# Kernel tuning notes

Hardware: AMD Instinct MI355X
Metric: run time of the kernel (lower is better)

Reference implementation:

```python
import jax, jax.numpy as jnp
import numpy as np

N, E, IN_DIM, H, OUT, MAPD = 20000, 640000, 24, 128, 24, 512
SLOPE = 0.01  # torch F.leaky_relu default


def setup_inputs() -> dict:
    key = jax.random.key(0)
    ks = jax.random.split(key, 20)
    g = lambda i, shape, s: jax.random.normal(ks[i], shape, jnp.float32) * s
    inp = {
        "feats": g(0, (N, IN_DIM), 1.0),
        "e_w": jax.random.uniform(ks[1], (E, 1), dtype=jnp.float32),
        "maps_embedding": g(2, (N, MAPD), 1.0),
        "snorm_n": jnp.ones((N, 1), jnp.float32),
        "src": jax.random.randint(ks[3], (E,), 0, N),
        "dst": jax.random.randint(ks[4], (E,), 0, N),
        "W_eh": g(5, (H, IN_DIM), (2.0 / IN_DIM) ** 0.5), "b_eh": jnp.zeros((H,), jnp.float32),
        "W_ee": g(6, (H, 1), 1.0), "b_ee": jnp.zeros((H,), jnp.float32),
        "W_cat": g(7, (H, H + MAPD), (2.0 / (H + MAPD)) ** 0.5), "b_cat": jnp.zeros((H,), jnp.float32),
        "Ws1": g(8, (H, H), (2.0 / H) ** 0.5), "Wf1": g(9, (H, H), (2.0 / H) ** 0.5),
        "a1": g(10, (2 * H,), (2.0 / (2 * H)) ** 0.5),
        "Ws2": g(11, (H, H), (2.0 / H) ** 0.5), "Wf2": g(12, (H, H), (2.0 / H) ** 0.5),
        "a2": g(13, (2 * H,), (2.0 / (2 * H)) ** 0.5),
        "W_out": g(14, (OUT, H), (2.0 / H) ** 0.5), "b_out": jnp.zeros((OUT,), jnp.float32),
    }
    return inp


def gat_layer(h, src, dst, Ws, Wf, a):
    # My_GATLayer with (as constructed in My_GAT) relu=False, att_ew=False, dropouts=0.
    h_in = h
    h_s = h @ Ws.T                         # [N,H] self transform
    z = h @ Wf.T                           # [N,H] message transform
    # attention score = leaky_relu(a^T [z_src, z_dst]) computed via per-node halves
    s_src = z @ a[:H]                      # [N]
    s_dst = z @ a[H:]                      # [N]
    e = jax.nn.leaky_relu(s_src[src] + s_dst[dst], SLOPE)          # [E]
    # numerically stable segment softmax over incoming edges grouped by dst
    m = jax.ops.segment_max(e, dst, num_segments=N)
    m = jnp.where(jnp.isfinite(m), m, 0.0)
    ex = jnp.exp(e - m[dst])
    denom = jax.ops.segment_sum(ex, dst, num_segments=N)
    alpha = ex / jnp.maximum(denom[dst], 1e-16)                    # [E]
    agg = jax.ops.segment_sum(alpha[:, None] * z[src], dst, num_segments=N)  # [N,H]
    indeg = jax.ops.segment_sum(jnp.ones_like(e), dst, num_segments=N)
    # DGL update_all leaves zero-in-degree nodes at their prior ndata['h'] (= h_in)
    h_node = jnp.where(indeg[:, None] > 0, h_s + agg, h_in)
    return h_in + h_node                   # residual connection; relu disabled (positional-arg bug)


def reference(feats, e_w, maps_embedding, snorm_n, src, dst,
              W_eh, b_eh, W_ee, b_ee, W_cat, b_cat,
              Ws1, Wf1, a1, Ws2, Wf2, a2, W_out, b_out):
    feats = feats.reshape(feats.shape[0], -1)
    h = feats @ W_eh.T + b_eh                                  # embedding_h
    _e = e_w @ W_ee.T + b_ee                                   # edge embedding (stored on g.edata['w'], unused since att_ew binds to attn_drop)
    h = jnp.concatenate([maps_embedding, h], axis=-1) @ W_cat.T + b_cat
    h = jax.nn.relu(h)
    h = gat_layer(h, src, dst, Ws1, Wf1, a1)
    h = gat_layer(h, src, dst, Ws2, Wf2, a2)
    return h @ W_out.T + b_out
```

## Files before the change

### kernel.cpp

```cpp
#include <hip/hip_runtime.h>

#define HBLK 128
#define EPB 4096

typedef __attribute__((ext_vector_type(8))) short s8v;
typedef __attribute__((ext_vector_type(4))) float f32x4;
typedef __attribute__((ext_vector_type(8))) _Float16 h8f;

__device__ inline void split2(float x, short& h, short& l) {
    unsigned hb = __float_as_uint(x) & 0xFFFF0000u;
    float hf = __uint_as_float(hb);
    float lf = x - hf;
    h = (short)(hb >> 16);
    l = (short)(__float_as_uint(lf) >> 16);
}

__device__ inline void split8(const float4& a0, const float4& a1, s8v& ah, s8v& al) {
    float vv[8];
    *(float4*)&vv[0] = a0;
    *(float4*)&vv[4] = a1;
#pragma unroll
    for (int e = 0; e < 8; ++e) {
        short hh, ll;
        split2(vv[e], hh, ll);
        ah[e] = hh;
        al[e] = ll;
    }
}


__global__ void bin_hist(const int* __restrict__ dst, int* __restrict__ histT,
                         int E, int NB1) {
    __shared__ int h[256];
    const int t = threadIdx.x, blk = blockIdx.x;
    h[t] = 0;
    __syncthreads();
    const int e0 = blk * EPB;
    const int e1 = min(E, e0 + EPB);
    for (int e = e0 + t; e < e1; e += 256)
        atomicAdd(&h[dst[e] >> 7], 1);
    __syncthreads();
    histT[t * NB1 + blk] = h[t];
}

__global__ void scan1(const int* __restrict__ counts, int* __restrict__ offs,
                      int* __restrict__ bsums, int n) {
    __shared__ int lds[256];
    const int t = threadIdx.x;
    const int i = blockIdx.x * 256 + t;
    const int v = (i < n) ? counts[i] : 0;
    lds[t] = v;
    __syncthreads();
    for (int off = 1; off < 256; off <<= 1) {
        int add = (t >= off) ? lds[t - off] : 0;
        __syncthreads();
        lds[t] += add;
        __syncthreads();
    }
    if (i < n) offs[i] = lds[t] - v;
    if (t == 255) bsums[blockIdx.x] = lds[255];
}

__global__ void scan2(int* __restrict__ bsums, int nb) {
    __shared__ int lds[256];
    const int t = threadIdx.x;
    const int v = (t < nb) ? bsums[t] : 0;
    lds[t] = v;
    __syncthreads();
    for (int off = 1; off < 256; off <<= 1) {
        int add = (t >= off) ? lds[t - off] : 0;
        __syncthreads();
        lds[t] += add;
        __syncthreads();
    }
    if (t < nb) bsums[t] = lds[t] - v;
}

__global__ void bin_scatter(const int* __restrict__ src, const int* __restrict__ dst,
                            const int* __restrict__ histT, const int* __restrict__ bsums,
                            int* __restrict__ ebuf, int E, int NB1) {
    __shared__ int cur[256];
    const int t = threadIdx.x, blk = blockIdx.x;
    const int li = t * NB1 + blk;
    cur[t] = histT[li] + bsums[li >> 8];
    __syncthreads();
    const int e0 = blk * EPB;
    const int e1 = min(E, e0 + EPB);
    for (int e = e0 + t; e < e1; e += 256) {
        const int d = dst[e];
        const int p = atomicAdd(&cur[d >> 7], 1);
        ebuf[p] = (src[e] << 7) | (d & 127);
    }
}

__global__ void bucket_sort(const int* __restrict__ ebuf, const int* __restrict__ histT,
                            const int* __restrict__ bsums,
                            int* __restrict__ offs, int* __restrict__ srcs,
                            int N, int E, int NB1) {
    __shared__ int cnt[256];
    __shared__ int cur[256];
    const int t = threadIdx.x, b = blockIdx.x;
    const int li0 = b * NB1;
    const int ebase = histT[li0] + bsums[li0 >> 8];
    int eend = E;
    if (b + 1 < 256) {
        const int li1 = (b + 1) * NB1;
        eend = histT[li1] + bsums[li1 >> 8];
    }
    cnt[t] = 0;
    __syncthreads();
    for (int e = ebase + t; e < eend; e += 256)
        atomicAdd(&cnt[ebuf[e] & 127], 1);
    __syncthreads();
    const int own = cnt[t];
    for (int off = 1; off < 256; off <<= 1) {
        int add = (t >= off) ? cnt[t - off] : 0;
        __syncthreads();
        cnt[t] += add;
        __syncthreads();
    }
    const int excl = cnt[t] - own;
    cur[t] = ebase + excl;
    const int node = (b << 7) + t;
    if (t < 128 && node < N) offs[node] = ebase + excl;
    if (b == 0 && t == 0) offs[N] = E;
    __syncthreads();
    for (int e = ebase + t; e < eend; e += 256) {
        const int ed = ebuf[e];
        const int p = atomicAdd(&cur[ed & 127], 1);
        srcs[p] = ed >> 7;
    }
}

__global__ void pack_all(const float* __restrict__ W0, const float* __restrict__ W1,
                         const float* __restrict__ W2, const float* __restrict__ W3,
                         short* __restrict__ dh, short* __restrict__ dl,
                         const float* __restrict__ Wcat, int ldw, int mapd,
                         const float* __restrict__ Weh, int indim,
                         const float* __restrict__ beh, const float* __restrict__ bcat,
                         short* __restrict__ ch, short* __restrict__ cl,
                         float* __restrict__ bcomb, int K) {
    const int m = blockIdx.y;
    const long i = (long)blockIdx.x * 256 + threadIdx.x;
    if (m < 4) {
        if (blockIdx.x >= 64) return;
        const float* Ws[4] = {W0, W1, W2, W3};
        const int c = (int)(i >> 7), k = (int)(i & 127);
        float x = Ws[m][c * HBLK + k];
        short h, l;
        split2(x, h, l);
        const int j = c >> 4, l16 = c & 15;
        const int chunk = k >> 5, quad = (k >> 3) & 3, t = k & 7;
        const long off = (long)m * 16384 + (((long)(chunk * 8 + j) * 64) + quad * 16 + l16) * 8 + t;
        dh[off] = h;
        dl[off] = l;
    } else {
        const long total = (long)HBLK * K;
        if (i < total) {
            const int c = (int)(i / K), k = (int)(i % K);
            float x = 0.f;
            if (k < mapd) {
                x = Wcat[(long)c * ldw + k];
            } else if (k < mapd + indim) {
                const float* wc = Wcat + (long)c * ldw + mapd;
                const int kk = k - mapd;
                float s = 0.f;
                for (int j = 0; j < HBLK; ++j) s += wc[j] * Weh[j * indim + kk];
                x = s;
            }
            short h, l;
            split2(x, h, l);
            const int j = c >> 4, l16 = c & 15;
            const int chunk = k >> 5, quad = (k >> 3) & 3, t = k & 7;
            const long off = (((long)(chunk * 8 + j) * 64) + quad * 16 + l16) * 8 + t;
            ch[off] = h;
            cl[off] = l;
        } else if (i < total + HBLK) {
            const int c = (int)(i - total);
            const float* wc = Wcat + (long)c * ldw + mapd;
            float s = bcat[c];
            for (int j = 0; j < HBLK; ++j) s += wc[j] * beh[j];
            bcomb[c] = s;
        }
    }
}

__global__ __launch_bounds__(256, 2) void gemm_bigk(
    const float* __restrict__ A1, int lda1, int K1,
    const float* __restrict__ A2, int lda2, int Kin,
    int K,
    const short* __restrict__ Wh, const short* __restrict__ Wl,
    const float* __restrict__ bias,
    float* __restrict__ Cf, int M)
{
    __shared__ short lds_h[2][4096];
    __shared__ short lds_l[2][4096];
    const int tid = threadIdx.x;
    const int wv = tid >> 6;
    const int lane = tid & 63;
    const int l16 = lane & 15;
    const int quad = lane >> 4;
    const int m0 = blockIdx.x * 64 + wv * 16;
    int ra = m0 + l16;
    if (ra >= M) ra = M - 1;
    const long r1 = (long)ra * lda1;
    const long r2 = (long)ra * lda2;
    const int NC = K >> 5;

    f32x4 acc[8];
#pragma unroll
    for (int j = 0; j < 8; ++j) acc[j] = (f32x4){0.f, 0.f, 0.f, 0.f};

#define LOAD_A(d0, d1, kb)                                      \
    {                                                           \
        const int col0 = (kb) + quad * 8;                       \
        if (col0 < K1) {                                        \
            const float* ap = A1 + r1 + col0;                   \
            d0 = *(const float4*)ap;                            \
            d1 = *(const float4*)(ap + 4);                      \
        } else if (col0 < Kin) {                                \
            const float* ap = A2 + r2 + (col0 - K1);            \
            d0 = *(const float4*)ap;                            \
            d1 = *(const float4*)(ap + 4);                      \
        } else {                                                \
            d0 = make_float4(0.f, 0.f, 0.f, 0.f);               \
            d1 = make_float4(0.f, 0.f, 0.f, 0.f);               \
        }                                                       \
    }
#define LOAD_W(r0, r1w, r2w, r3, c)                             \
    {                                                           \
        const int4* gh = (const int4*)(Wh + (long)(c) * 4096);  \
        const int4* gl = (const int4*)(Wl + (long)(c) * 4096);  \
        r0 = gh[tid * 2]; r1w = gh[tid * 2 + 1];                \
        r2w = gl[tid * 2]; r3 = gl[tid * 2 + 1];                \
    }
#define WRITE_W(b, r0, r1w, r2w, r3)                            \
    {                                                           \
        int4* bh = (int4*)lds_h[b];                             \
        int4* bl = (int4*)lds_l[b];                             \
        bh[tid * 2] = r0; bh[tid * 2 + 1] = r1w;                \
        bl[tid * 2] = r2w; bl[tid * 2 + 1] = r3;                \
    }

    int4 wa0, wa1, wa2, wa3, wb0, wb1, wb2, wb3;
    LOAD_W(wa0, wa1, wa2, wa3, 0)
    WRITE_W(0, wa0, wa1, wa2, wa3)
    LOAD_W(wa0, wa1, wa2, wa3, 1)
    LOAD_W(wb0, wb1, wb2, wb3, 2)
    float4 a0c, a1c, a0n, a1n, a0p, a1p;
    float4 a0q = make_float4(0.f, 0.f, 0.f, 0.f);
    float4 a1q = make_float4(0.f, 0.f, 0.f, 0.f);
    LOAD_A(a0c, a1c, 0)
    LOAD_A(a0n, a1n, 32)
    LOAD_A(a0p, a1p, 64)
    asm volatile("s_waitcnt lgkmcnt(0)" ::: "memory");
    __builtin_amdgcn_s_barrier();
    asm volatile("" ::: "memory");

    for (int c = 0; c < NC; ++c) {
        const int nb = c & 1;
        if (c + 3 < NC) {
            LOAD_A(a0q, a1q, (c + 3) * 32)
        }
        s8v ah, al;
        split8(a0c, a1c, ah, al);
#pragma unroll
        for (int j = 0; j < 8; ++j) {
            const s8v whf = *(const s8v*)&lds_h[nb][(j * 64 + lane) * 8];
            const s8v wlf = *(const s8v*)&lds_l[nb][(j * 64 + lane) * 8];
            acc[j] = __builtin_amdgcn_mfma_f32_16x16x32_bf16(ah, whf, acc[j], 0, 0, 0);
            acc[j] = __builtin_amdgcn_mfma_f32_16x16x32_bf16(ah, wlf, acc[j], 0, 0, 0);
            acc[j] = __builtin_amdgcn_mfma_f32_16x16x32_bf16(al, whf, acc[j], 0, 0, 0);
        }
        if (c + 1 < NC) {
            WRITE_W(nb ^ 1, wa0, wa1, wa2, wa3)
            wa0 = wb0; wa1 = wb1; wa2 = wb2; wa3 = wb3;
            if (c + 3 < NC) LOAD_W(wb0, wb1, wb2, wb3, c + 3)
            asm volatile("s_waitcnt lgkmcnt(0)" ::: "memory");
            __builtin_amdgcn_s_barrier();
            asm volatile("" ::: "memory");
        }
        a0c = a0n; a1c = a1n;
        a0n = a0p; a1n = a1p;
        a0p = a0q; a1p = a1q;
    }
#undef LOAD_A
#undef LOAD_W
#undef WRITE_W

#pragma unroll
    for (int r = 0; r < 4; ++r) {
        const int gr = m0 + quad * 4 + r;
        if (gr >= M) continue;
#pragma unroll
        for (int j = 0; j < 8; ++j) {
            const int col = j * 16 + l16;
            float v = acc[j][r] + bias[col];
            Cf[(long)gr * HBLK + col] = fmaxf(v, 0.f);
        }
    }
}

__global__ __launch_bounds__(256, 2) void gemm_layer(
    const float* __restrict__ A,
    const short* __restrict__ Wsh, const short* __restrict__ Wsl,
    const short* __restrict__ Wfh, const short* __restrict__ Wfl,
    float* __restrict__ hsOut, _Float16* __restrict__ zOut,
    const float* __restrict__ avec,
    float* __restrict__ sOut, float* __restrict__ dOut, int M)
{
    __shared__ short lh[16384];
    __shared__ short ll[16384];
    const int tid = threadIdx.x;
    const int wv = tid >> 6;
    const int lane = tid & 63;
    const int l16 = lane & 15;
    const int quad = lane >> 4;
    const int m0 = blockIdx.x * 64 + wv * 16;
    int ra = m0 + l16;
    if (ra >= M) ra = M - 1;
    const float* arow = A + (long)ra * HBLK + quad * 8;

    {
        const int4* gh = (const int4*)Wfh;
        const int4* gl = (const int4*)Wfl;
        int4* bh = (int4*)lh;
        int4* bl = (int4*)ll;
#pragma unroll
        for (int i = 0; i < 8; ++i) {
            bh[i * 256 + tid] = gh[i * 256 + tid];
            bl[i * 256 + tid] = gl[i * 256 + tid];
        }
    }
    float4 aw0[4], aw1[4];
#pragma unroll
    for (int c = 0; c < 4; ++c) {
        aw0[c] = *(const float4*)(arow + c * 32);
        aw1[c] = *(const float4*)(arow + c * 32 + 4);
    }
    int4 wsh[8], wsl[8];
    {
        const int4* gh = (const int4*)Wsh;
        const int4* gl = (const int4*)Wsl;
#pragma unroll
        for (int i = 0; i < 8; ++i) {
            wsh[i] = gh[i * 256 + tid];
            wsl[i] = gl[i * 256 + tid];
        }
    }
    s8v ahf[4], alf[4];
#pragma unroll
    for (int c = 0; c < 4; ++c) split8(aw0[c], aw1[c], ahf[c], alf[c]);

    f32x4 acc[8];
#pragma unroll
    for (int j = 0; j < 8; ++j) acc[j] = (f32x4){0.f, 0.f, 0.f, 0.f};
    asm volatile("s_waitcnt lgkmcnt(0)" ::: "memory");
    __builtin_amdgcn_s_barrier();
    asm volatile("" ::: "memory");

#pragma unroll
    for (int c = 0; c < 4; ++c) {
#pragma unroll
        for (int j = 0; j < 8; ++j) {
            const s8v whf = *(const s8v*)&lh[((c * 8 + j) * 64 + lane) * 8];
            const s8v wlf = *(const s8v*)&ll[((c * 8 + j) * 64 + lane) * 8];
            acc[j] = __builtin_amdgcn_mfma_f32_16x16x32_bf16(ahf[c], whf, acc[j], 0, 0, 0);
            acc[j] = __builtin_amdgcn_mfma_f32_16x16x32_bf16(ahf[c], wlf, acc[j], 0, 0, 0);
            acc[j] = __builtin_amdgcn_mfma_f32_16x16x32_bf16(alf[c], whf, acc[j], 0, 0, 0);
        }
    }
#pragma unroll
    for (int r = 0; r < 4; ++r) {
        const int gr = m0 + quad * 4 + r;
        if (gr >= M) continue;
#pragma unroll
        for (int j = 0; j < 8; ++j)
            zOut[(long)gr * HBLK + j * 16 + l16] = (_Float16)acc[j][r];
    }
    {
        float av0[8], av1[8];
#pragma unroll
        for (int j = 0; j < 8; ++j) {
            av0[j] = avec[j * 16 + l16];
            av1[j] = avec[128 + j * 16 + l16];
        }
#pragma unroll
        for (int r = 0; r < 4; ++r) {
            float ssp = 0.f, sdp = 0.f;
#pragma unroll
            for (int j = 0; j < 8; ++j) {
                const float v = acc[j][r];
                ssp += v * av0[j];
                sdp += v * av1[j];
            }
#pragma unroll
            for (int off = 1; off < 16; off <<= 1) {
                ssp += __shfl_xor(ssp, off);
                sdp += __shfl_xor(sdp, off);
            }
            const int gr = m0 + quad * 4 + r;
            if (l16 == 0 && gr < M) {
                sOut[gr] = ssp;
                dOut[gr] = sdp;
            }
        }
    }

    asm volatile("s_waitcnt lgkmcnt(0)" ::: "memory");
    __builtin_amdgcn_s_barrier();
    asm volatile("" ::: "memory");
    {
        int4* bh = (int4*)lh;
        int4* bl = (int4*)ll;
#pragma unroll
        for (int i = 0; i < 8; ++i) {
            bh[i * 256 + tid] = wsh[i];
            bl[i * 256 + tid] = wsl[i];
        }
    }
    asm volatile("s_waitcnt lgkmcnt(0)" ::: "memory");
    __builtin_amdgcn_s_barrier();
    asm volatile("" ::: "memory");

#pragma unroll
    for (int j = 0; j < 8; ++j) acc[j] = (f32x4){0.f, 0.f, 0.f, 0.f};
#pragma unroll
    for (int c = 0; c < 4; ++c) {
#pragma unroll
        for (int j = 0; j < 8; ++j) {
            const s8v whf = *(const s8v*)&lh[((c * 8 + j) * 64 + lane) * 8];
            const s8v wlf = *(const s8v*)&ll[((c * 8 + j) * 64 + lane) * 8];
            acc[j] = __builtin_amdgcn_mfma_f32_16x16x32_bf16(ahf[c], whf, acc[j], 0, 0, 0);
            acc[j] = __builtin_amdgcn_mfma_f32_16x16x32_bf16(ahf[c], wlf, acc[j], 0, 0, 0);
            acc[j] = __builtin_amdgcn_mfma_f32_16x16x32_bf16(alf[c], whf, acc[j], 0, 0, 0);
        }
    }
#pragma unroll
    for (int r = 0; r < 4; ++r) {
        const int gr = m0 + quad * 4 + r;
        if (gr >= M) continue;
#pragma unroll
        for (int j = 0; j < 8; ++j)
            hsOut[(long)gr * HBLK + j * 16 + l16] = acc[j][r];
    }
}

template <int FOUT>
__global__ void gat_gather(const float* __restrict__ h_in, const float* __restrict__ hs,
                           const _Float16* __restrict__ zh,
                           const float* __restrict__ s_src, const float* __restrict__ s_dst,
                           const int* __restrict__ offs, const int* __restrict__ srcs,
                           float* __restrict__ h_out,
                           const float* __restrict__ Wout, const float* __restrict__ bout,
                           float* __restrict__ outp, int OUTD, int N) {
    __shared__ float wlds[FOUT ? (32 * 132 + 4 * 132) : 4];
    const int tid = threadIdx.x;
    const int wave = tid >> 6;
    const int lane = tid & 63;
    if constexpr (FOUT) {
        for (int i = tid; i < OUTD * HBLK; i += 256)
            wlds[(i >> 7) * 132 + (i & 127)] = Wout[i];
        __syncthreads();
    }
    const int n = blockIdx.x * 4 + wave;
    if (n >= N) return;
    const int g = lane >> 4, l = lane & 15;
    const int beg = offs[n], end = offs[n + 1];
    const int deg = end - beg;

    float acc[8] = {};
    if (deg > 0) {
        const float sd = s_dst[n];
        if (deg <= 64) {
            const int sA = srcs[beg + min(lane, deg - 1)];
            float e = sd + s_src[sA];
            e = e > 0.f ? e : 0.01f * e;
            if (lane >= deg) e = -INFINITY;
            float mv = e;
#pragma unroll
            for (int off = 32; off; off >>= 1) mv = fmaxf(mv, __shfl_xor(mv, off));
            const float ex = (lane < deg) ? __expf(e - mv) : 0.f;
            float sv = ex;
#pragma unroll
            for (int off = 32; off; off >>= 1) sv += __shfl_xor(sv, off);
            const float w = ex / fmaxf(sv, 1e-16f);

            const int nK = (deg + 3) >> 2;
            int k = 0;
            for (; k + 1 < nK; k += 2) {
                const int i0 = 4 * k + g;
                const int i1 = i0 + 4;
                const int s0 = __shfl(sA, i0);
                const int s1 = __shfl(sA, i1);
                const float w0 = __shfl(w, i0);
                const float w1 = __shfl(w, i1);
                const h8f z0 = *(const h8f*)(zh + (long)s0 * HBLK + 8 * l);
                const h8f z1 = *(const h8f*)(zh + (long)s1 * HBLK + 8 * l);
#pragma unroll
                for (int e2 = 0; e2 < 8; ++e2)
                    acc[e2] += w0 * (float)z0[e2] + w1 * (float)z1[e2];
            }
            if (k < nK) {
                const int i0 = 4 * k + g;
                const int s0 = __shfl(sA, i0);
                const float w0 = __shfl(w, i0);
                const h8f z0 = *(const h8f*)(zh + (long)s0 * HBLK + 8 * l);
#pragma unroll
                for (int e2 = 0; e2 < 8; ++e2)
                    acc[e2] += w0 * (float)z0[e2];
            }
        } else {
            float m = -INFINITY, s = 0.f;
            for (int i = beg + lane; i < end; i += 64) {
                float e = sd + s_src[srcs[i]];
                e = e > 0.f ? e : 0.01f * e;
                float nm = fmaxf(m, e);
                s = s * __expf(m - nm) + __expf(e - nm);
                m = nm;
            }
#pragma unroll
            for (int off = 32; off > 0; off >>= 1) {
                float m2 = __shfl_down(m, off);
                float s2 = __shfl_down(s, off);
                if (m2 > m) {
                    float t = m; m = m2; m2 = t;
                    float ts = s; s = s2; s2 = ts;
                }
                s = (m == -INFINITY) ? 0.f : s + s2 * __expf(m2 - m);
            }
            m = __shfl(m, 0);
            s = __shfl(s, 0);
            const float inv = 1.f / fmaxf(s, 1e-16f);
            for (int i = beg + g; i < end; i += 4) {
                const int s0 = srcs[i];
                float e0 = sd + s_src[s0];
                e0 = e0 > 0.f ? e0 : 0.01f * e0;
                const float w0 = __expf(e0 - m) * inv;
                const h8f z0 = *(const h8f*)(zh + (long)s0 * HBLK + 8 * l);
#pragma unroll
                for (int e2 = 0; e2 < 8; ++e2)
                    acc[e2] += w0 * (float)z0[e2];
            }
        }
#pragma unroll
        for (int e2 = 0; e2 < 8; ++e2) {
            acc[e2] += __shfl_down(acc[e2], 32);
            acc[e2] += __shfl_down(acc[e2], 16);
        }
    }

    if (g == 0) {
        const long base = (long)n * HBLK + 8 * l;
        const float4 hi0 = *(const float4*)(h_in + base);
        const float4 hi1 = *(const float4*)(h_in + base + 4);
        float o[8];
        if (deg > 0) {
            const float4 hv0 = *(const float4*)(hs + base);
            const float4 hv1 = *(const float4*)(hs + base + 4);
            const float* hip = (const float*)&hi0;
            const float* hvp = (const float*)&hv0;
#pragma unroll
            for (int e = 0; e < 4; ++e) o[e] = hip[e] + hvp[e] + acc[e];
            const float* hip1 = (const float*)&hi1;
            const float* hvp1 = (const float*)&hv1;
#pragma unroll
            for (int e = 0; e < 4; ++e) o[4 + e] = hip1[e] + hvp1[e] + acc[4 + e];
        } else {
            const float* hip = (const float*)&hi0;
            const float* hip1 = (const float*)&hi1;
#pragma unroll
            for (int e = 0; e < 4; ++e) o[e] = 2.f * hip[e];
#pragma unroll
            for (int e = 0; e < 4; ++e) o[4 + e] = 2.f * hip1[e];
        }
        if constexpr (FOUT) {
            float* hr = wlds + 32 * 132 + wave * 132;
            *(float4*)&hr[8 * l] = *(float4*)&o[0];
            *(float4*)&hr[8 * l + 4] = *(float4*)&o[4];
        } else {
            *(float4*)(h_out + base) = *(float4*)&o[0];
            *(float4*)(h_out + base + 4) = *(float4*)&o[4];
        }
    }
    if constexpr (FOUT) {
        if (lane < OUTD) {
            const float* hr = wlds + 32 * 132 + wave * 132;
            const float* wr = wlds + lane * 132;
            float a = bout[lane];
#pragma unroll 8
            for (int k = 0; k < 32; ++k) {
                const float4 hv = *(const float4*)&hr[k * 4];
                const float4 wv = *(const float4*)&wr[k * 4];
                a += hv.x * wv.x + hv.y * wv.y + hv.z * wv.z + hv.w * wv.w;
            }
            outp[(long)n * OUTD + lane] = a;
        }
    }
}

extern "C" void kernel_launch(void* const* d_in, const int* in_sizes, int n_in,
                              void* d_out, int out_size, void* d_ws, size_t ws_size,
                              hipStream_t stream) {
    const float* feats = (const float*)d_in[0];
    const float* maps  = (const float*)d_in[2];
    const int* src = (const int*)d_in[4];
    const int* dst = (const int*)d_in[5];
    const float* W_eh  = (const float*)d_in[6];
    const float* b_eh  = (const float*)d_in[7];
    const float* W_cat = (const float*)d_in[10];
    const float* b_cat = (const float*)d_in[11];
    const float* Ws1 = (const float*)d_in[12];
    const float* Wf1 = (const float*)d_in[13];
    const float* a1  = (const float*)d_in[14];
    const float* Ws2 = (const float*)d_in[15];
    const float* Wf2 = (const float*)d_in[16];
    const float* a2  = (const float*)d_in[17];
    const float* W_out = (const float*)d_in[18];
    const float* b_out = (const float*)d_in[19];

    const int N = in_sizes[3];
    const int E = in_sizes[4];
    const int IN_DIM = in_sizes[0] / N;
    const int MAPD = in_sizes[2] / N;
    const int OUTD = in_sizes[19];
    const int KCAT = MAPD + HBLK;
    const int KC = (MAPD + IN_DIM + 31) & ~31;

    char* p = (char*)d_ws;
    const size_t NH = (size_t)N * HBLK;
    float* hin  = (float*)p;  p += NH * 4;
    float* hs   = (float*)p;  p += NH * 4;
    float* hout = (float*)p;  p += NH * 4;
    _Float16* zh = (_Float16*)p; p += NH * 2;
    float* ssrc = (float*)p;  p += (size_t)N * 4;
    float* sdst = (float*)p;  p += (size_t)N * 4;
    int* offs   = (int*)p;    p += (size_t)(N + 1) * 4;
    int* srcs   = (int*)p;    p += (size_t)E * 4;
    int* bsums  = (int*)p;    p += 256 * 4;
    int* histT  = (int*)p;    p += (size_t)256 * 256 * 4;
    float* bcomb = (float*)p; p += (size_t)HBLK * 4;
    p = (char*)(((uintptr_t)p + 15) & ~(uintptr_t)15);
    int* ebuf = (int*)p;      p += (size_t)E * 4;
    short* Wcat_h = (short*)p; p += (size_t)HBLK * KC * 2;
    short* Wcat_l = (short*)p; p += (size_t)HBLK * KC * 2;
    short* Wly_h = (short*)p;  p += (size_t)4 * HBLK * HBLK * 2;
    short* Wly_l = (short*)p;  p += (size_t)4 * HBLK * HBLK * 2;

    const int NB1 = (E + EPB - 1) / EPB;
    const int NBUCK = (N + 127) >> 7;
    const int nHist = 256 * NB1;
    bin_hist<<<NB1, 256, 0, stream>>>(dst, histT, E, NB1);
    scan1<<<NB1, 256, 0, stream>>>(histT, histT, bsums, nHist);
    scan2<<<1, 256, 0, stream>>>(bsums, NB1);
    bin_scatter<<<NB1, 256, 0, stream>>>(src, dst, histT, bsums, ebuf, E, NB1);
    bucket_sort<<<NBUCK, 256, 0, stream>>>(ebuf, histT, bsums, offs, srcs, N, E, NB1);

    const int nbW = (HBLK * KC + HBLK + 255) / 256;
    pack_all<<<dim3(nbW, 5), 256, 0, stream>>>(
        Ws1, Wf1, Ws2, Wf2, Wly_h, Wly_l,
        W_cat, KCAT, MAPD, W_eh, IN_DIM, b_eh, b_cat, Wcat_h, Wcat_l, bcomb, KC);

    const int gGrid = (N + 63) / 64;
    const int n4 = (N + 3) / 4;

    gemm_bigk<<<gGrid, 256, 0, stream>>>(
        maps, MAPD, MAPD, feats, IN_DIM, MAPD + IN_DIM, KC,
        Wcat_h, Wcat_l, bcomb, hin, N);

    gemm_layer<<<gGrid, 256, 0, stream>>>(
        hin, Wly_h, Wly_l, Wly_h + 16384, Wly_l + 16384,
        hs, zh, a1, ssrc, sdst, N);
    gat_gather<0><<<n4, 256, 0, stream>>>(hin, hs, zh, ssrc, sdst, offs, srcs, hout,
                                          nullptr, nullptr, nullptr, OUTD, N);

    gemm_layer<<<gGrid, 256, 0, stream>>>(
        hout, Wly_h + 32768, Wly_l + 32768, Wly_h + 49152, Wly_l + 49152,
        hs, zh, a2, ssrc, sdst, N);
    gat_gather<1><<<n4, 256, 0, stream>>>(hout, hs, zh, ssrc, sdst, offs, srcs, nullptr,
                                          W_out, b_out, (float*)d_out, OUTD, N);
}
```

Baseline: 261.2 us.

## Merge CSR build and weight packing into one cooperative kernel with grid syncs

Replaces the five CSR-construction kernels and the weight-pack kernel with a single cooperative launch of 256 blocks that uses grid.sync between phases. Weight packing runs in the blocks not needed for the histogram, so the two overlap. This removes several kernel launches and their gaps, at the cost of grid-wide barriers and a fixed grid of 256 blocks that must all be co-resident.

```diff
diff --git a/kernel.cpp b/kernel.cpp
--- a/kernel.cpp
+++ b/kernel.cpp
@@ -1,4 +1,7 @@
 #include <hip/hip_runtime.h>
+#include <hip/hip_cooperative_groups.h>
+
+namespace cg = cooperative_groups;
 
 #define HBLK 128
 #define EPB 4096
@@ -29,158 +32,157 @@
 }
 
 
-__global__ void bin_hist(const int* __restrict__ dst, int* __restrict__ histT,
-                         int E, int NB1) {
-    __shared__ int h[256];
+struct CoopArgs {
+    const int* src; const int* dst;
+    int* histT; int* bsums; int* ebuf; int* offs; int* srcs;
+    int E; int N; int NB1; int NBUCK;
+    const float* W0; const float* W1; const float* W2; const float* W3;
+    short* dh; short* dl;
+    const float* Wcat; int ldw; int mapd;
+    const float* Weh; int indim;
+    const float* beh; const float* bcat;
+    short* ch; short* cl; float* bcomb; int K;
+};
+
+__global__ __launch_bounds__(256, 1) void csr_pack_coop(CoopArgs a) {
+    cg::grid_group grid = cg::this_grid();
+    __shared__ int sh0[256];
+    __shared__ int sh1[256];
     const int t = threadIdx.x, blk = blockIdx.x;
-    h[t] = 0;
-    __syncthreads();
-    const int e0 = blk * EPB;
-    const int e1 = min(E, e0 + EPB);
-    for (int e = e0 + t; e < e1; e += 256)
-        atomicAdd(&h[dst[e] >> 7], 1);
-    __syncthreads();
-    histT[t * NB1 + blk] = h[t];
-}
-
-__global__ void scan1(const int* __restrict__ counts, int* __restrict__ offs,
-                      int* __restrict__ bsums, int n) {
-    __shared__ int lds[256];
-    const int t = threadIdx.x;
-    const int i = blockIdx.x * 256 + t;
-    const int v = (i < n) ? counts[i] : 0;
-    lds[t] = v;
-    __syncthreads();
-    for (int off = 1; off < 256; off <<= 1) {
-        int add = (t >= off) ? lds[t - off] : 0;
-        __syncthreads();
-        lds[t] += add;
-        __syncthreads();
-    }
-    if (i < n) offs[i] = lds[t] - v;
-    if (t == 255) bsums[blockIdx.x] = lds[255];
-}
-
-__global__ void scan2(int* __restrict__ bsums, int nb) {
-    __shared__ int lds[256];
-    const int t = threadIdx.x;
-    const int v = (t < nb) ? bsums[t] : 0;
-    lds[t] = v;
-    __syncthreads();
-    for (int off = 1; off < 256; off <<= 1) {
-        int add = (t >= off) ? lds[t - off] : 0;
-        __syncthreads();
-        lds[t] += add;
-        __syncthreads();
-    }
-    if (t < nb) bsums[t] = lds[t] - v;
-}
-
-__global__ void bin_scatter(const int* __restrict__ src, const int* __restrict__ dst,
-                            const int* __restrict__ histT, const int* __restrict__ bsums,
-                            int* __restrict__ ebuf, int E, int NB1) {
-    __shared__ int cur[256];
-    const int t = threadIdx.x, blk = blockIdx.x;
-    const int li = t * NB1 + blk;
-    cur[t] = histT[li] + bsums[li >> 8];
-    __syncthreads();
-    const int e0 = blk * EPB;
-    const int e1 = min(E, e0 + EPB);
-    for (int e = e0 + t; e < e1; e += 256) {
-        const int d = dst[e];
-        const int p = atomicAdd(&cur[d >> 7], 1);
-        ebuf[p] = (src[e] << 7) | (d & 127);
-    }
-}
-
-__global__ void bucket_sort(const int* __restrict__ ebuf, const int* __restrict__ histT,
-                            const int* __restrict__ bsums,
-                            int* __restrict__ offs, int* __restrict__ srcs,
-                            int N, int E, int NB1) {
-    __shared__ int cnt[256];
-    __shared__ int cur[256];
-    const int t = threadIdx.x, b = blockIdx.x;
-    const int li0 = b * NB1;
-    const int ebase = histT[li0] + bsums[li0 >> 8];
-    int eend = E;
-    if (b + 1 < 256) {
-        const int li1 = (b + 1) * NB1;
-        eend = histT[li1] + bsums[li1 >> 8];
-    }
-    cnt[t] = 0;
-    __syncthreads();
-    for (int e = ebase + t; e < eend; e += 256)
-        atomicAdd(&cnt[ebuf[e] & 127], 1);
-    __syncthreads();
-    const int own = cnt[t];
-    for (int off = 1; off < 256; off <<= 1) {
-        int add = (t >= off) ? cnt[t - off] : 0;
-        __syncthreads();
-        cnt[t] += add;
-        __syncthreads();
-    }
-    const int excl = cnt[t] - own;
-    cur[t] = ebase + excl;
-    const int node = (b << 7) + t;
-    if (t < 128 && node < N) offs[node] = ebase + excl;
-    if (b == 0 && t == 0) offs[N] = E;
-    __syncthreads();
-    for (int e = ebase + t; e < eend; e += 256) {
-        const int ed = ebuf[e];
-        const int p = atomicAdd(&cur[ed & 127], 1);
-        srcs[p] = ed >> 7;
-    }
-}
-
-__global__ void pack_all(const float* __restrict__ W0, const float* __restrict__ W1,
-                         const float* __restrict__ W2, const float* __restrict__ W3,
-                         short* __restrict__ dh, short* __restrict__ dl,
-                         const float* __restrict__ Wcat, int ldw, int mapd,
-                         const float* __restrict__ Weh, int indim,
-                         const float* __restrict__ beh, const float* __restrict__ bcat,
-                         short* __restrict__ ch, short* __restrict__ cl,
-                         float* __restrict__ bcomb, int K) {
-    const int m = blockIdx.y;
-    const long i = (long)blockIdx.x * 256 + threadIdx.x;
-    if (m < 4) {
-        if (blockIdx.x >= 64) return;
-        const float* Ws[4] = {W0, W1, W2, W3};
-        const int c = (int)(i >> 7), k = (int)(i & 127);
-        float x = Ws[m][c * HBLK + k];
-        short h, l;
-        split2(x, h, l);
-        const int j = c >> 4, l16 = c & 15;
-        const int chunk = k >> 5, quad = (k >> 3) & 3, t = k & 7;
-        const long off = (long)m * 16384 + (((long)(chunk * 8 + j) * 64) + quad * 16 + l16) * 8 + t;
-        dh[off] = h;
-        dl[off] = l;
+
+    if (blk < a.NB1) {
+        sh0[t] = 0;
+        __syncthreads();
+        const int e0 = blk * EPB, e1 = min(a.E, e0 + EPB);
+        for (int e = e0 + t; e < e1; e += 256)
+            atomicAdd(&sh0[a.dst[e] >> 7], 1);
+        __syncthreads();
+        a.histT[t * a.NB1 + blk] = sh0[t];
     } else {
-        const long total = (long)HBLK * K;
-        if (i < total) {
-            const int c = (int)(i / K), k = (int)(i % K);
-            float x = 0.f;
-            if (k < mapd) {
-                x = Wcat[(long)c * ldw + k];
-            } else if (k < mapd + indim) {
-                const float* wc = Wcat + (long)c * ldw + mapd;
-                const int kk = k - mapd;
-                float s = 0.f;
-                for (int j = 0; j < HBLK; ++j) s += wc[j] * Weh[j * indim + kk];
-                x = s;
-            }
-            short h, l;
-            split2(x, h, l);
-            const int j = c >> 4, l16 = c & 15;
-            const int chunk = k >> 5, quad = (k >> 3) & 3, t = k & 7;
-            const long off = (((long)(chunk * 8 + j) * 64) + quad * 16 + l16) * 8 + t;
-            ch[off] = h;
-            cl[off] = l;
-        } else if (i < total + HBLK) {
-            const int c = (int)(i - total);
-            const float* wc = Wcat + (long)c * ldw + mapd;
-            float s = bcat[c];
-            for (int j = 0; j < HBLK; ++j) s += wc[j] * beh[j];
-            bcomb[c] = s;
+        const int pb = blk - a.NB1, npb = 256 - a.NB1;
+        const long tw = 65536 + (long)HBLK * a.K + HBLK;
+        for (long idx = (long)pb * 256 + t; idx < tw; idx += (long)npb * 256) {
+            if (idx < 65536) {
+                const int m = (int)(idx >> 14);
+                const long i = idx & 16383;
+                const float* W = (m == 0) ? a.W0 : (m == 1) ? a.W1 : (m == 2) ? a.W2 : a.W3;
+                const int c = (int)(i >> 7), k = (int)(i & 127);
+                float x = W[c * HBLK + k];
+                short h, l;
+                split2(x, h, l);
+                const int j = c >> 4, l16 = c & 15;
+                const int chunk = k >> 5, quad = (k >> 3) & 3, tt = k & 7;
+                const long off = (long)m * 16384 +
+                                 (((long)(chunk * 8 + j) * 64) + quad * 16 + l16) * 8 + tt;
+                a.dh[off] = h;
+                a.dl[off] = l;
+            } else {
+                const long i = idx - 65536;
+                const long total = (long)HBLK * a.K;
+                if (i < total) {
+                    const int c = (int)(i / a.K), k = (int)(i % a.K);
+                    float x = 0.f;
+                    if (k < a.mapd) {
+                        x = a.Wcat[(long)c * a.ldw + k];
+                    } else if (k < a.mapd + a.indim) {
+                        const float* wc = a.Wcat + (long)c * a.ldw + a.mapd;
+                        const int kk = k - a.mapd;
+                        float s = 0.f;
+                        for (int j = 0; j < HBLK; ++j) s += wc[j] * a.Weh[j * a.indim + kk];
+                        x = s;
+                    }
+                    short h, l;
+                    split2(x, h, l);
+                    const int j = c >> 4, l16 = c & 15;
+                    const int chunk = k >> 5, quad = (k >> 3) & 3, tt = k & 7;
+                    const long off = (((long)(chunk * 8 + j) * 64) + quad * 16 + l16) * 8 + tt;
+                    a.ch[off] = h;
+                    a.cl[off] = l;
+                } else {
+                    const int c = (int)(i - total);
+                    const float* wc = a.Wcat + (long)c * a.ldw + a.mapd;
+                    float s = a.bcat[c];
+                    for (int j = 0; j < HBLK; ++j) s += wc[j] * a.beh[j];
+                    a.bcomb[c] = s;
+                }
+            }
+        }
+    }
+    grid.sync();
+
+    if (blk < a.NB1) {
+        const int i = blk * 256 + t;
+        const int v = a.histT[i];
+        sh0[t] = v;
+        __syncthreads();
+        for (int off = 1; off < 256; off <<= 1) {
+            int add = (t >= off) ? sh0[t - off] : 0;
+            __syncthreads();
+            sh0[t] += add;
+            __syncthreads();
+        }
+        a.histT[i] = sh0[t] - v;
+        if (t == 255) a.bsums[blk] = sh0[255];
+    }
+    grid.sync();
+
+    if (blk == 0) {
+        const int v = (t < a.NB1) ? a.bsums[t] : 0;
+        sh0[t] = v;
+        __syncthreads();
+        for (int off = 1; off < 256; off <<= 1) {
+            int add = (t >= off) ? sh0[t - off] : 0;
+            __syncthreads();
+            sh0[t] += add;
+            __syncthreads();
+        }
+        if (t < a.NB1) a.bsums[t] = sh0[t] - v;
+    }
+    grid.sync();
+
+    if (blk < a.NB1) {
+        const int li = t * a.NB1 + blk;
+        sh0[t] = a.histT[li] + a.bsums[li >> 8];
+        __syncthreads();
+        const int e0 = blk * EPB, e1 = min(a.E, e0 + EPB);
+        for (int e = e0 + t; e < e1; e += 256) {
+            const int d = a.dst[e];
+            const int p = atomicAdd(&sh0[d >> 7], 1);
+            a.ebuf[p] = (a.src[e] << 7) | (d & 127);
+        }
+    }
+    grid.sync();
+
+    if (blk < a.NBUCK) {
+        const int li0 = blk * a.NB1;
+        const int ebase = a.histT[li0] + a.bsums[li0 >> 8];
+        int eend = a.E;
+        if (blk + 1 < 256) {
+            const int li1 = (blk + 1) * a.NB1;
+            eend = a.histT[li1] + a.bsums[li1 >> 8];
+        }
+        sh0[t] = 0;
+        __syncthreads();
+        for (int e = ebase + t; e < eend; e += 256)
+            atomicAdd(&sh0[a.ebuf[e] & 127], 1);
+        __syncthreads();
+        const int own = sh0[t];
+        for (int off = 1; off < 256; off <<= 1) {
+            int add = (t >= off) ? sh0[t - off] : 0;
+            __syncthreads();
+            sh0[t] += add;
+            __syncthreads();
+        }
+        const int excl = sh0[t] - own;
+        sh1[t] = ebase + excl;
+        const int node = (blk << 7) + t;
+        if (t < 128 && node < a.N) a.offs[node] = ebase + excl;
+        if (blk == 0 && t == 0) a.offs[a.N] = a.E;
+        __syncthreads();
+        for (int e = ebase + t; e < eend; e += 256) {
+            const int ed = a.ebuf[e];
+            const int p = atomicAdd(&sh1[ed & 127], 1);
+            a.srcs[p] = ed >> 7;
         }
     }
 }
@@ -649,17 +651,19 @@
 
     const int NB1 = (E + EPB - 1) / EPB;
     const int NBUCK = (N + 127) >> 7;
-    const int nHist = 256 * NB1;
-    bin_hist<<<NB1, 256, 0, stream>>>(dst, histT, E, NB1);
-    scan1<<<NB1, 256, 0, stream>>>(histT, histT, bsums, nHist);
-    scan2<<<1, 256, 0, stream>>>(bsums, NB1);
-    bin_scatter<<<NB1, 256, 0, stream>>>(src, dst, histT, bsums, ebuf, E, NB1);
-    bucket_sort<<<NBUCK, 256, 0, stream>>>(ebuf, histT, bsums, offs, srcs, N, E, NB1);
-
-    const int nbW = (HBLK * KC + HBLK + 255) / 256;
-    pack_all<<<dim3(nbW, 5), 256, 0, stream>>>(
-        Ws1, Wf1, Ws2, Wf2, Wly_h, Wly_l,
-        W_cat, KCAT, MAPD, W_eh, IN_DIM, b_eh, b_cat, Wcat_h, Wcat_l, bcomb, KC);
+    CoopArgs ca;
+    ca.src = src; ca.dst = dst;
+    ca.histT = histT; ca.bsums = bsums; ca.ebuf = ebuf; ca.offs = offs; ca.srcs = srcs;
+    ca.E = E; ca.N = N; ca.NB1 = NB1; ca.NBUCK = NBUCK;
+    ca.W0 = Ws1; ca.W1 = Wf1; ca.W2 = Ws2; ca.W3 = Wf2;
+    ca.dh = Wly_h; ca.dl = Wly_l;
+    ca.Wcat = W_cat; ca.ldw = KCAT; ca.mapd = MAPD;
+    ca.Weh = W_eh; ca.indim = IN_DIM;
+    ca.beh = b_eh; ca.bcat = b_cat;
+    ca.ch = Wcat_h; ca.cl = Wcat_l; ca.bcomb = bcomb; ca.K = KC;
+    void* coopArgs[] = {&ca};
+    hipLaunchCooperativeKernel((const void*)csr_pack_coop, dim3(256), dim3(256),
+                               coopArgs, 0, stream);
 
     const int gGrid = (N + 63) / 64;
     const int n4 = (N + 3) / 4;
```

New measurement: 410.7 us. 57.2% more time.

## Shrink gemm_bigk blocks to 128 threads with 32-row tiles

Applied to the files above, without the earlier changes.

The big-K concat GEMM now launches 128-thread blocks covering 32 rows instead of 256 threads covering 64 rows, doubling the grid. Each thread now loads twice as many weight vectors per chunk, and the weight prefetch pipeline drops from two chunks ahead to one. The intent is more blocks in flight and better latency hiding across CUs. In exchange, each block re-streams the same weight chunks for half as many rows, so weight traffic roughly doubles and the shallower prefetch may expose load latency.

```diff
diff --git a/kernel.cpp b/kernel.cpp
--- a/kernel.cpp
+++ b/kernel.cpp
@@ -185,7 +185,7 @@
     }
 }
 
-__global__ __launch_bounds__(256, 2) void gemm_bigk(
+__global__ __launch_bounds__(128, 2) void gemm_bigk(
     const float* __restrict__ A1, int lda1, int K1,
     const float* __restrict__ A2, int lda2, int Kin,
     int K,
@@ -200,7 +200,7 @@
     const int lane = tid & 63;
     const int l16 = lane & 15;
     const int quad = lane >> 4;
-    const int m0 = blockIdx.x * 64 + wv * 16;
+    const int m0 = blockIdx.x * 32 + wv * 16;
     int ra = m0 + l16;
     if (ra >= M) ra = M - 1;
     const long r1 = (long)ra * lda1;
@@ -227,26 +227,29 @@
             d1 = make_float4(0.f, 0.f, 0.f, 0.f);               \
         }                                                       \
     }
-#define LOAD_W(r0, r1w, r2w, r3, c)                             \
+#define LOAD_W(c)                                               \
     {                                                           \
         const int4* gh = (const int4*)(Wh + (long)(c) * 4096);  \
         const int4* gl = (const int4*)(Wl + (long)(c) * 4096);  \
-        r0 = gh[tid * 2]; r1w = gh[tid * 2 + 1];                \
-        r2w = gl[tid * 2]; r3 = gl[tid * 2 + 1];                \
-    }
-#define WRITE_W(b, r0, r1w, r2w, r3)                            \
+        wh0 = gh[tid * 4];     wh1 = gh[tid * 4 + 1];           \
+        wh2 = gh[tid * 4 + 2]; wh3 = gh[tid * 4 + 3];           \
+        wl0 = gl[tid * 4];     wl1 = gl[tid * 4 + 1];           \
+        wl2 = gl[tid * 4 + 2]; wl3 = gl[tid * 4 + 3];           \
+    }
+#define WRITE_W(b)                                              \
     {                                                           \
         int4* bh = (int4*)lds_h[b];                             \
         int4* bl = (int4*)lds_l[b];                             \
-        bh[tid * 2] = r0; bh[tid * 2 + 1] = r1w;                \
-        bl[tid * 2] = r2w; bl[tid * 2 + 1] = r3;                \
-    }
-
-    int4 wa0, wa1, wa2, wa3, wb0, wb1, wb2, wb3;
-    LOAD_W(wa0, wa1, wa2, wa3, 0)
-    WRITE_W(0, wa0, wa1, wa2, wa3)
-    LOAD_W(wa0, wa1, wa2, wa3, 1)
-    LOAD_W(wb0, wb1, wb2, wb3, 2)
+        bh[tid * 4] = wh0;     bh[tid * 4 + 1] = wh1;           \
+        bh[tid * 4 + 2] = wh2; bh[tid * 4 + 3] = wh3;           \
+        bl[tid * 4] = wl0;     bl[tid * 4 + 1] = wl1;           \
+        bl[tid * 4 + 2] = wl2; bl[tid * 4 + 3] = wl3;           \
+    }
+
+    int4 wh0, wh1, wh2, wh3, wl0, wl1, wl2, wl3;
+    LOAD_W(0)
+    WRITE_W(0)
+    LOAD_W(1)
     float4 a0c, a1c, a0n, a1n, a0p, a1p;
     float4 a0q = make_float4(0.f, 0.f, 0.f, 0.f);
     float4 a1q = make_float4(0.f, 0.f, 0.f, 0.f);
@@ -273,9 +276,8 @@
             acc[j] = __builtin_amdgcn_mfma_f32_16x16x32_bf16(al, whf, acc[j], 0, 0, 0);
         }
         if (c + 1 < NC) {
-            WRITE_W(nb ^ 1, wa0, wa1, wa2, wa3)
-            wa0 = wb0; wa1 = wb1; wa2 = wb2; wa3 = wb3;
-            if (c + 3 < NC) LOAD_W(wb0, wb1, wb2, wb3, c + 3)
+            WRITE_W(nb ^ 1)
+            if (c + 2 < NC) LOAD_W(c + 2)
             asm volatile("s_waitcnt lgkmcnt(0)" ::: "memory");
             __builtin_amdgcn_s_barrier();
             asm volatile("" ::: "memory");
@@ -661,10 +663,11 @@
         Ws1, Wf1, Ws2, Wf2, Wly_h, Wly_l,
         W_cat, KCAT, MAPD, W_eh, IN_DIM, b_eh, b_cat, Wcat_h, Wcat_l, bcomb, KC);
 
+    const int gGridB = (N + 31) / 32;
     const int gGrid = (N + 63) / 64;
     const int n4 = (N + 3) / 4;
 
-    gemm_bigk<<<gGrid, 256, 0, stream>>>(
+    gemm_bigk<<<gGridB, 128, 0, stream>>>(
         maps, MAPD, MAPD, feats, IN_DIM, MAPD + IN_DIM, KC,
         Wcat_h, Wcat_l, bcomb, hin, N);
 
```

New measurement: 259.1 us. No clear change (-0.8%).
